# Performance work log

Measured on AMD Instinct MI355X. Metric: run time of the kernel, lower is better.

## Reference

```python
import jax, jax.numpy as jnp
import numpy as np

D_MODEL = 1024
N_HEADS = 16
D_HEAD = 64
D_FF = 4096
WINDOW = 256
B, T = 2, 2048


def setup_inputs() -> dict:
    key = jax.random.key(0)
    ks = jax.random.split(key, 10)
    tot = N_HEADS * D_HEAD
    def w(k, shape):
        # approximate kaiming_normal_ fan_out init: std = sqrt(2/fan_out)
        fan_out = shape[0]
        return jax.random.normal(k, shape, jnp.float32) * np.sqrt(2.0 / fan_out)
    return {
        "x": jax.random.normal(ks[0], (B, T, D_MODEL), jnp.float32),
        "ln1_w": jnp.ones((D_MODEL,), jnp.float32),
        "qkv_w": w(ks[1], (3 * tot, D_MODEL)),
        "gate_w": w(ks[2], (tot, D_MODEL)),
        "out_w": w(ks[3], (D_MODEL, tot)),
        "ln2_w": jnp.ones((D_MODEL,), jnp.float32),
        "wg": w(ks[4], (D_FF, D_MODEL)),
        "wu": w(ks[5], (D_FF, D_MODEL)),
        "wo": w(ks[6], (D_MODEL, D_FF)),
    }


def _rmsnorm(x, w):
    return x * jax.lax.rsqrt(jnp.mean(x * x, axis=-1, keepdims=True) + 1e-6) * w


def _attention(x, qkv_w, gate_w, out_w):
    Bq, Tq, _ = x.shape
    tot = N_HEADS * D_HEAD
    qkv = x @ qkv_w.T  # [B,T,3*tot]
    q, k, v = jnp.split(qkv, 3, axis=-1)
    q = q.reshape(Bq, Tq, N_HEADS, D_HEAD).transpose(0, 2, 1, 3)
    k = k.reshape(Bq, Tq, N_HEADS, D_HEAD).transpose(0, 2, 1, 3)
    v = v.reshape(Bq, Tq, N_HEADS, D_HEAD).transpose(0, 2, 1, 3)
    scale = D_HEAD ** -0.5
    scores = jnp.einsum("bhqd,bhkd->bhqk", q, k) * scale
    pos = jnp.arange(Tq)
    dist = pos[:, None] - pos[None, :]
    allowed = (dist >= 0) & (dist < WINDOW)  # causal sliding window
    mask = jnp.where(allowed, 0.0, -jnp.inf).astype(scores.dtype)
    attn = jax.nn.softmax(scores + mask[None, None], axis=-1)
    out = jnp.einsum("bhqk,bhkd->bhqd", attn, v)
    out = out.transpose(0, 2, 1, 3).reshape(Bq, Tq, tot)
    gate = jax.nn.sigmoid(x @ gate_w.T)
    return (out * gate) @ out_w.T


def reference(x, ln1_w, qkv_w, gate_w, out_w, ln2_w, wg, wu, wo):
    x = x + _attention(_rmsnorm(x, ln1_w), qkv_w, gate_w, out_w)
    h = _rmsnorm(x, ln2_w)
    ffn = (jax.nn.silu(h @ wg.T) * (h @ wu.T)) @ wo.T
    return x + ffn
```

## Files before the change

kernel.cpp:

```cpp
#include <hip/hip_runtime.h>


#define DEV __device__ __forceinline__

using u16 = unsigned short;
typedef __attribute__((ext_vector_type(8))) short  short8;
typedef __attribute__((ext_vector_type(4))) float  floatx4;

DEV u16 f2bf(float f) {
  unsigned u = __builtin_bit_cast(unsigned, f);
  u += 0x7FFFu + ((u >> 16) & 1u);
  return (u16)(u >> 16);
}
DEV float bf2f(u16 h) {
  unsigned u = ((unsigned)h) << 16;
  return __builtin_bit_cast(float, u);
}
DEV floatx4 mfma16(short8 a, short8 b, floatx4 c) {
  return __builtin_amdgcn_mfma_f32_16x16x32_bf16(a, b, c, 0, 0, 0);
}
DEV void gload16(const u16* g, const char* lds_base_wave_uniform) {
  __builtin_amdgcn_global_load_lds(
      (const __attribute__((address_space(1))) void*)g,
      (__attribute__((address_space(3))) void*)lds_base_wave_uniform,
      16, 0, 0);
}
#define WAITVM(n) asm volatile("s_waitcnt vmcnt(" #n ")" ::: "memory")
DEV void blockbar() {
  asm volatile("" ::: "memory");
  __builtin_amdgcn_s_barrier();
  asm volatile("" ::: "memory");
}

__global__ __launch_bounds__(256) void cvt_all_k(
    const float* __restrict__ s0, const float* __restrict__ s1,
    const float* __restrict__ s2, const float* __restrict__ s3,
    const float* __restrict__ s4, const float* __restrict__ s5,
    u16* __restrict__ d0, u16* __restrict__ d1, u16* __restrict__ d2,
    u16* __restrict__ d3, u16* __restrict__ d4, u16* __restrict__ d5) {
  const int b = blockIdx.x;
  const float* in; u16* out; int base;
  if (b < 3072)       { in = s0; out = d0; base = 0; }
  else if (b < 4096)  { in = s1; out = d1; base = 3072; }
  else if (b < 5120)  { in = s2; out = d2; base = 4096; }
  else if (b < 9216)  { in = s3; out = d3; base = 5120; }
  else if (b < 13312) { in = s4; out = d4; base = 9216; }
  else                { in = s5; out = d5; base = 13312; }
  const size_t i = (size_t)(b - base) * 256 + threadIdx.x;
  const float4 v = ((const float4*)in)[i];
  ushort4 r;
  r.x = f2bf(v.x); r.y = f2bf(v.y); r.z = f2bf(v.z); r.w = f2bf(v.w);
  ((ushort4*)out)[i] = r;
}

__global__ __launch_bounds__(256) void rmsnorm_k(const float* __restrict__ x,
                                                 const float* __restrict__ wt,
                                                 u16* __restrict__ o) {
  __shared__ float red[4];
  const int row = blockIdx.x;
  const int tid = threadIdx.x;
  const float4 v = ((const float4*)(x + (size_t)row * 1024))[tid];
  float ss = v.x * v.x + v.y * v.y + v.z * v.z + v.w * v.w;
  ss += __shfl_xor(ss, 1, 64);
  ss += __shfl_xor(ss, 2, 64);
  ss += __shfl_xor(ss, 4, 64);
  ss += __shfl_xor(ss, 8, 64);
  ss += __shfl_xor(ss, 16, 64);
  ss += __shfl_xor(ss, 32, 64);
  if ((tid & 63) == 0) red[tid >> 6] = ss;
  __syncthreads();
  const float tot = red[0] + red[1] + red[2] + red[3];
  const float sc = rsqrtf(tot * (1.0f / 1024.0f) + 1e-6f);
  const float4 wv = ((const float4*)wt)[tid];
  ushort4 r;
  r.x = f2bf(v.x * sc * wv.x);
  r.y = f2bf(v.y * sc * wv.y);
  r.z = f2bf(v.z * sc * wv.z);
  r.w = f2bf(v.w * sc * wv.w);
  ((ushort4*)(o + (size_t)row * 1024))[tid] = r;
}

template <int CFG, int EPI>
__global__ __launch_bounds__((CFG == 0) ? 512 : 256, 2) void gemm8p(
    const u16* __restrict__ Ag, const u16* __restrict__ Bg, int N, int K,
    u16* __restrict__ cb, float* __restrict__ cf,
    const u16* __restrict__ aux, const float* __restrict__ resid,
    u16* __restrict__ cb2) {
  constexpr int BM = (CFG == 0) ? 256 : 128;
  constexpr int NWAVES = (CFG == 0) ? 8 : 4;
  constexpr int WAVES_N = (CFG == 0) ? 4 : 2;
  constexpr int WM = (CFG == 0) ? 128 : 64;
  constexpr int NI = WM / 16;
  constexpr int NJ = 4;
  constexpr int IH = (CFG == 0) ? NI / 2 : NI;
  constexpr int GB = BM * 64;
  constexpr int BUFB = 4 * GB;
  __shared__ __align__(16) char lds[2 * BUFB];

  const int tid = threadIdx.x;
  const int w = tid >> 6, lane = tid & 63;
  const int wm = w / WAVES_N, wn = w % WAVES_N;
  const int g = lane >> 4, r16 = lane & 15;

  int bid = blockIdx.y * gridDim.x + blockIdx.x;
  const int cpx = (gridDim.x * gridDim.y) >> 3;
  bid = (bid & 7) * cpx + (bid >> 3);
  const int m0 = (bid / gridDim.x) * BM;
  const int n0 = (bid % gridDim.x) * BM;

  floatx4 acc[NI][NJ];
#pragma unroll
  for (int i = 0; i < NI; i++)
#pragma unroll
    for (int j = 0; j < NJ; j++) acc[i][j] = (floatx4){0.f, 0.f, 0.f, 0.f};

  const int nt = K >> 6;

  const int srow = w * 32 + (lane >> 2);
  const int scol8 = (lane & 3) * 8;
  auto stageG = [&](int G, int t) {
    if (t >= nt) return;
    const u16* Mat = (G < 2) ? Ag : Bg;
    const int base0 = (G < 2) ? m0 : n0;
    const int kc = t * 64 + (G & 1) * 32 + scol8;
    const char* dst = lds + (t & 1) * BUFB + G * GB + w * 2048;
#pragma unroll
    for (int q = 0; q < 2; q++)
      gload16(Mat + (size_t)(base0 + srow + q * 16) * K + kc, dst + q * 1024);
  };

  auto rdA = [&](short8* af, int ks, int ihalf, const char* buf) {
#pragma unroll
    for (int i = 0; i < IH; i++) {
      const int arow = wm * WM + (ihalf * IH + i) * 16 + r16;
      af[i] = *(const short8*)(buf + ks * GB + arow * 64 + g * 16);
    }
  };
  auto rdB = [&](short8* bf_, int ks, const char* buf) {
#pragma unroll
    for (int j = 0; j < NJ; j++) {
      const int brow = wn * 64 + j * 16 + r16;
      bf_[j] = *(const short8*)(buf + 2 * GB + ks * GB + brow * 64 + g * 16);
    }
  };
  auto mm = [&](short8* af, short8* bf_, int ihalf) {
    __builtin_amdgcn_s_setprio(1);
#pragma unroll
    for (int i = 0; i < IH; i++)
#pragma unroll
      for (int j = 0; j < NJ; j++)
        acc[ihalf * IH + i][j] = mfma16(af[i], bf_[j], acc[ihalf * IH + i][j]);
    __builtin_amdgcn_s_setprio(0);
  };

  if constexpr (CFG == 0) { stageG(1, 0); stageG(2, 0); stageG(0, 0); stageG(3, 0); }
  else                    { stageG(0, 0); stageG(2, 0); stageG(1, 0); stageG(3, 0); }

  for (int t = 0; t < nt; ++t) {
    const char* buf = lds + (t & 1) * BUFB;
    short8 af[IH], bfv[NJ];
    if constexpr (CFG == 0) {
      WAITVM(2);
      blockbar();
      rdA(af, 0, 0, buf); rdB(bfv, 0, buf);
      stageG(1, t + 1);
      mm(af, bfv, 0);
      blockbar();
      rdA(af, 0, 1, buf);
      stageG(2, t + 1);
      mm(af, bfv, 1);
      if (t + 1 < nt) { WAITVM(4); } else { WAITVM(0); }
      blockbar();
      rdA(af, 1, 0, buf); rdB(bfv, 1, buf);
      stageG(0, t + 1);
      mm(af, bfv, 0);
      blockbar();
      rdA(af, 1, 1, buf);
      stageG(3, t + 1);
      mm(af, bfv, 1);
    } else {
      WAITVM(4);
      blockbar();
      rdA(af, 0, 0, buf); rdB(bfv, 0, buf);
      stageG(0, t + 1); stageG(2, t + 1);
      mm(af, bfv, 0);
      if (t + 1 < nt) { WAITVM(4); } else { WAITVM(0); }
      blockbar();
      rdA(af, 1, 0, buf); rdB(bfv, 1, buf);
      stageG(1, t + 1); stageG(3, t + 1);
      mm(af, bfv, 0);
    }
  }

#pragma unroll
  for (int i = 0; i < NI; i++) {
    const int row = m0 + wm * WM + i * 16 + g * 4;
#pragma unroll
    for (int j = 0; j < NJ; j++) {
      const int col = n0 + wn * 64 + j * 16 + r16;
#pragma unroll
      for (int rr = 0; rr < 4; rr++) {
        const float v = acc[i][j][rr];
        if constexpr (EPI == 2) {
          cb[(size_t)(row + rr) * N + col] = f2bf(v / (1.0f + __expf(-v)));
        } else if constexpr (EPI == 3) {
          const size_t idx = (size_t)(row + rr) * N + col;
          cb[idx] = f2bf(v * bf2f(aux[idx]));
        } else if constexpr (EPI == 4) {
          const size_t idx = (size_t)(row + rr) * N + col;
          cf[idx] = v + resid[idx];
        } else if constexpr (EPI == 6) {
          if (col < 3072)
            cb[(size_t)(row + rr) * 3072 + col] = f2bf(v);
          else
            cb2[(size_t)(row + rr) * 1024 + (col - 3072)] =
                f2bf(1.0f / (1.0f + __expf(-v)));
        }
      }
    }
  }
}

__global__ __launch_bounds__(256) void attn_win_kernel(
    const u16* __restrict__ qkv, const u16* __restrict__ gate,
    u16* __restrict__ out) {
  __shared__ __align__(16) u16 Kl[64][80];
  __shared__ __align__(16) u16 Vt[64][80];
  __shared__ __align__(16) u16 Pl[4][16][80];

  const int tid = threadIdx.x;
  const int w = tid >> 6, lane = tid & 63;
  const int g = lane >> 4, r16 = lane & 15;

  const int q0 = blockIdx.x * 64;
  const int h = blockIdx.y;
  const int b = blockIdx.z;
  const u16* qb_ = qkv + (size_t)b * 2048 * 3072;

  const int tq = q0 + w * 16 + r16;
  const u16* qptr = qb_ + (size_t)tq * 3072 + h * 64;
  const short8 aq0 = *(const short8*)(qptr + g * 8);
  const short8 aq1 = *(const short8*)(qptr + 32 + g * 8);

  floatx4 O[4] = {{0,0,0,0},{0,0,0,0},{0,0,0,0},{0,0,0,0}};
  float mrow[4] = {-1e30f, -1e30f, -1e30f, -1e30f};
  float lrow[4] = {0.f, 0.f, 0.f, 0.f};

  const int srow = tid >> 2;
  const int sq4 = tid & 3;
  const int qw = q0 + w * 16;

  for (int kt = q0 - 256; kt <= q0; kt += 64) {
    if (kt < 0) continue;
    {
      const u16* kb = qb_ + (size_t)(kt + srow) * 3072 + 1024 + h * 64 + sq4 * 16;
      const short8 kv0 = *(const short8*)kb;
      const short8 kv1 = *(const short8*)(kb + 8);
      *(short8*)&Kl[srow][sq4 * 16] = kv0;
      *(short8*)&Kl[srow][sq4 * 16 + 8] = kv1;
      const u16* vb = kb + 1024;
      const short8 vv0 = *(const short8*)vb;
      const short8 vv1 = *(const short8*)(vb + 8);
#pragma unroll
      for (int j = 0; j < 8; j++) Vt[sq4 * 16 + j][srow] = (u16)vv0[j];
#pragma unroll
      for (int j = 0; j < 8; j++) Vt[sq4 * 16 + 8 + j][srow] = (u16)vv1[j];
    }
    __syncthreads();

    const bool active = (qw + 15 >= kt) && (qw - kt < 319);
    if (active) {
      floatx4 S[4];
#pragma unroll
      for (int nf = 0; nf < 4; nf++) {
        const short8 bk0 = *(const short8*)&Kl[nf * 16 + r16][g * 8];
        const short8 bk1 = *(const short8*)&Kl[nf * 16 + r16][32 + g * 8];
        floatx4 a = {0.f, 0.f, 0.f, 0.f};
        a = mfma16(aq0, bk0, a);
        a = mfma16(aq1, bk1, a);
        S[nf] = a;
      }
      float pm[4][4];
      float nmax[4] = {-1e30f, -1e30f, -1e30f, -1e30f};
#pragma unroll
      for (int nf = 0; nf < 4; nf++) {
        const int key = kt + nf * 16 + r16;
#pragma unroll
        for (int rr = 0; rr < 4; rr++) {
          const int q = qw + g * 4 + rr;
          const int dist = q - key;
          const float s = (dist >= 0 && dist < 256) ? S[nf][rr] : -1e30f;
          pm[nf][rr] = s;
          nmax[rr] = fmaxf(nmax[rr], s);
        }
      }
#pragma unroll
      for (int rr = 0; rr < 4; rr++) {
        float v = nmax[rr];
        v = fmaxf(v, __shfl_xor(v, 1, 64));
        v = fmaxf(v, __shfl_xor(v, 2, 64));
        v = fmaxf(v, __shfl_xor(v, 4, 64));
        v = fmaxf(v, __shfl_xor(v, 8, 64));
        const float mnew = fmaxf(mrow[rr], v);
        const float alpha = __expf(0.125f * (mrow[rr] - mnew));
        mrow[rr] = mnew;
        lrow[rr] *= alpha;
#pragma unroll
        for (int n = 0; n < 4; n++) O[n][rr] *= alpha;
        float ls = 0.f;
#pragma unroll
        for (int nf = 0; nf < 4; nf++) {
          const float s = pm[nf][rr];
          const float pv = (s < -1e29f) ? 0.f : __expf(0.125f * (s - mnew));
          pm[nf][rr] = pv;
          ls += pv;
        }
        ls += __shfl_xor(ls, 1, 64);
        ls += __shfl_xor(ls, 2, 64);
        ls += __shfl_xor(ls, 4, 64);
        ls += __shfl_xor(ls, 8, 64);
        lrow[rr] += ls;
      }
#pragma unroll
      for (int nf = 0; nf < 4; nf++)
#pragma unroll
        for (int rr = 0; rr < 4; rr++)
          Pl[w][g * 4 + rr][nf * 16 + r16] = f2bf(pm[nf][rr]);
#pragma unroll
      for (int kf = 0; kf < 2; kf++) {
        const short8 pa = *(const short8*)&Pl[w][r16][kf * 32 + g * 8];
#pragma unroll
        for (int n = 0; n < 4; n++) {
          const short8 vb8 = *(const short8*)&Vt[n * 16 + r16][kf * 32 + g * 8];
          O[n] = mfma16(pa, vb8, O[n]);
        }
      }
    }
    __syncthreads();
  }

#pragma unroll
  for (int n = 0; n < 4; n++) {
#pragma unroll
    for (int rr = 0; rr < 4; rr++) {
      const int t = qw + g * 4 + rr;
      const size_t idx = ((size_t)(b * 2048 + t)) * 1024 + h * 64 + n * 16 + r16;
      const float gv = bf2f(gate[idx]);
      const float ov = (O[n][rr] / lrow[rr]) * gv;
      out[idx] = f2bf(ov);
    }
  }
}

extern "C" void kernel_launch(void* const* d_in, const int* in_sizes, int n_in,
                              void* d_out, int out_size, void* d_ws,
                              size_t ws_size, hipStream_t stream) {
  (void)in_sizes; (void)n_in; (void)out_size; (void)ws_size;
  const float* x     = (const float*)d_in[0];
  const float* ln1   = (const float*)d_in[1];
  const float* qkvw  = (const float*)d_in[2];
  const float* gatew = (const float*)d_in[3];
  const float* outw  = (const float*)d_in[4];
  const float* ln2   = (const float*)d_in[5];
  const float* wg    = (const float*)d_in[6];
  const float* wu    = (const float*)d_in[7];
  const float* wo    = (const float*)d_in[8];
  float* outp = (float*)d_out;

  u16* p = (u16*)d_ws;
  u16* qkvw_b  = p; p += 3 * 1024 * 1024;
  u16* gatew_b = p; p += 1024 * 1024;
  u16* outw_b  = p; p += 1024 * 1024;
  u16* wg_b    = p; p += 4 * 1024 * 1024;
  u16* wu_b    = p; p += 4 * 1024 * 1024;
  u16* wo_b    = p; p += 4 * 1024 * 1024;
  u16* xn      = p; p += 4096 * 1024;
  u16* qkvb    = p; p += (size_t)4096 * 3072;
  u16* gates   = p; p += 4096 * 1024;
  u16* a3      = p; p += 4096 * 1024;
  u16* hb      = p; p += 4096 * 1024;
  u16* gs      = p; p += (size_t)4096 * 4096;
  float* x2    = (float*)p;

  cvt_all_k<<<17408, 256, 0, stream>>>(qkvw, gatew, outw, wg, wu, wo,
                                       qkvw_b, gatew_b, outw_b, wg_b, wu_b, wo_b);

  rmsnorm_k<<<4096, 256, 0, stream>>>(x, ln1, xn);

  gemm8p<0, 6><<<dim3(16, 16), 512, 0, stream>>>(
      xn, qkvw_b, 4096, 1024, qkvb, nullptr, nullptr, nullptr, gates);

  attn_win_kernel<<<dim3(32, 16, 2), 256, 0, stream>>>(qkvb, gates, a3);

  gemm8p<1, 4><<<dim3(8, 32), 256, 0, stream>>>(
      a3, outw_b, 1024, 1024, nullptr, x2, nullptr, x, nullptr);

  rmsnorm_k<<<4096, 256, 0, stream>>>(x2, ln2, hb);

  gemm8p<0, 2><<<dim3(16, 16), 512, 0, stream>>>(
      hb, wg_b, 4096, 1024, gs, nullptr, nullptr, nullptr, nullptr);
  gemm8p<0, 3><<<dim3(16, 16), 512, 0, stream>>>(
      hb, wu_b, 4096, 1024, gs, nullptr, gs, nullptr, nullptr);

  gemm8p<1, 4><<<dim3(8, 32), 256, 0, stream>>>(
      gs, wo_b, 1024, 4096, nullptr, outp, nullptr, x2, nullptr);
}
```

Before: 364.7 us.

## Swizzle GEMM LDS layout and use 8 waves for 128-tile config

Applies an XOR swizzle to the k-group column of LDS tiles for both staging writes and fragment reads, to cut LDS bank conflicts in the MFMA operand loads. The 128x128 GEMM config now runs 8 waves (512 threads), each owning a 64x32 sub-tile. Staging is reorganised so each wave loads 16 rows per pass, and the vmcnt waits and stage order are adjusted to match. More waves per tile aim to hide latency better, at the cost of fewer accumulators per wave and more staging instructions per byte.

```diff
diff --git a/kernel.cpp b/kernel.cpp
--- a/kernel.cpp
+++ b/kernel.cpp
@@ -81,26 +81,27 @@
 }
 
 template <int CFG, int EPI>
-__global__ __launch_bounds__((CFG == 0) ? 512 : 256, 2) void gemm8p(
+__global__ __launch_bounds__(512, 2) void gemm8p(
     const u16* __restrict__ Ag, const u16* __restrict__ Bg, int N, int K,
     u16* __restrict__ cb, float* __restrict__ cf,
     const u16* __restrict__ aux, const float* __restrict__ resid,
     u16* __restrict__ cb2) {
   constexpr int BM = (CFG == 0) ? 256 : 128;
-  constexpr int NWAVES = (CFG == 0) ? 8 : 4;
-  constexpr int WAVES_N = (CFG == 0) ? 4 : 2;
   constexpr int WM = (CFG == 0) ? 128 : 64;
+  constexpr int WN = (CFG == 0) ? 64 : 32;
   constexpr int NI = WM / 16;
-  constexpr int NJ = 4;
+  constexpr int NJ = WN / 16;
   constexpr int IH = (CFG == 0) ? NI / 2 : NI;
   constexpr int GB = BM * 64;
+  constexpr int QI = (CFG == 0) ? 2 : 1;
   constexpr int BUFB = 4 * GB;
   __shared__ __align__(16) char lds[2 * BUFB];
 
   const int tid = threadIdx.x;
   const int w = tid >> 6, lane = tid & 63;
-  const int wm = w / WAVES_N, wn = w % WAVES_N;
+  const int wm = w >> 2, wn = w & 3;
   const int g = lane >> 4, r16 = lane & 15;
+  const int gx = (g ^ ((r16 >> 1) & 3)) << 4;
 
   int bid = blockIdx.y * gridDim.x + blockIdx.x;
   const int cpx = (gridDim.x * gridDim.y) >> 3;
@@ -116,31 +117,32 @@
 
   const int nt = K >> 6;
 
-  const int srow = w * 32 + (lane >> 2);
-  const int scol8 = (lane & 3) * 8;
+  const int kg_src = (lane & 3) ^ ((lane >> 3) & 3);
   auto stageG = [&](int G, int t) {
     if (t >= nt) return;
     const u16* Mat = (G < 2) ? Ag : Bg;
-    const int base0 = (G < 2) ? m0 : n0;
-    const int kc = t * 64 + (G & 1) * 32 + scol8;
-    const char* dst = lds + (t & 1) * BUFB + G * GB + w * 2048;
-#pragma unroll
-    for (int q = 0; q < 2; q++)
-      gload16(Mat + (size_t)(base0 + srow + q * 16) * K + kc, dst + q * 1024);
+    const int b0 = (G < 2) ? m0 : n0;
+    const int kc = t * 64 + (G & 1) * 32 + kg_src * 8;
+    const char* dst = lds + (t & 1) * BUFB + G * GB + w * 1024;
+#pragma unroll
+    for (int q = 0; q < QI; q++) {
+      const int row = q * 128 + w * 16 + (lane >> 2);
+      gload16(Mat + (size_t)(b0 + row) * K + kc, dst + q * 8192);
+    }
   };
 
   auto rdA = [&](short8* af, int ks, int ihalf, const char* buf) {
 #pragma unroll
     for (int i = 0; i < IH; i++) {
       const int arow = wm * WM + (ihalf * IH + i) * 16 + r16;
-      af[i] = *(const short8*)(buf + ks * GB + arow * 64 + g * 16);
+      af[i] = *(const short8*)(buf + ks * GB + arow * 64 + gx);
     }
   };
   auto rdB = [&](short8* bf_, int ks, const char* buf) {
 #pragma unroll
     for (int j = 0; j < NJ; j++) {
-      const int brow = wn * 64 + j * 16 + r16;
-      bf_[j] = *(const short8*)(buf + 2 * GB + ks * GB + brow * 64 + g * 16);
+      const int brow = wn * WN + j * 16 + r16;
+      bf_[j] = *(const short8*)(buf + 2 * GB + ks * GB + brow * 64 + gx);
     }
   };
   auto mm = [&](short8* af, short8* bf_, int ihalf) {
@@ -153,17 +155,16 @@
     __builtin_amdgcn_s_setprio(0);
   };
 
-  if constexpr (CFG == 0) { stageG(1, 0); stageG(2, 0); stageG(0, 0); stageG(3, 0); }
-  else                    { stageG(0, 0); stageG(2, 0); stageG(1, 0); stageG(3, 0); }
+  stageG(0, 0); stageG(2, 0); stageG(1, 0); stageG(3, 0);
 
   for (int t = 0; t < nt; ++t) {
     const char* buf = lds + (t & 1) * BUFB;
     short8 af[IH], bfv[NJ];
     if constexpr (CFG == 0) {
-      WAITVM(2);
+      WAITVM(4);
       blockbar();
       rdA(af, 0, 0, buf); rdB(bfv, 0, buf);
-      stageG(1, t + 1);
+      stageG(0, t + 1);
       mm(af, bfv, 0);
       blockbar();
       rdA(af, 0, 1, buf);
@@ -172,19 +173,19 @@
       if (t + 1 < nt) { WAITVM(4); } else { WAITVM(0); }
       blockbar();
       rdA(af, 1, 0, buf); rdB(bfv, 1, buf);
-      stageG(0, t + 1);
+      stageG(1, t + 1);
       mm(af, bfv, 0);
       blockbar();
       rdA(af, 1, 1, buf);
       stageG(3, t + 1);
       mm(af, bfv, 1);
     } else {
-      WAITVM(4);
+      WAITVM(2);
       blockbar();
       rdA(af, 0, 0, buf); rdB(bfv, 0, buf);
       stageG(0, t + 1); stageG(2, t + 1);
       mm(af, bfv, 0);
-      if (t + 1 < nt) { WAITVM(4); } else { WAITVM(0); }
+      if (t + 1 < nt) { WAITVM(2); } else { WAITVM(0); }
       blockbar();
       rdA(af, 1, 0, buf); rdB(bfv, 1, buf);
       stageG(1, t + 1); stageG(3, t + 1);
@@ -197,7 +198,7 @@
     const int row = m0 + wm * WM + i * 16 + g * 4;
 #pragma unroll
     for (int j = 0; j < NJ; j++) {
-      const int col = n0 + wn * 64 + j * 16 + r16;
+      const int col = n0 + wn * WN + j * 16 + r16;
 #pragma unroll
       for (int rr = 0; rr < 4; rr++) {
         const float v = acc[i][j][rr];
@@ -392,7 +393,7 @@
 
   attn_win_kernel<<<dim3(32, 16, 2), 256, 0, stream>>>(qkvb, gates, a3);
 
-  gemm8p<1, 4><<<dim3(8, 32), 256, 0, stream>>>(
+  gemm8p<1, 4><<<dim3(8, 32), 512, 0, stream>>>(
       a3, outw_b, 1024, 1024, nullptr, x2, nullptr, x, nullptr);
 
   rmsnorm_k<<<4096, 256, 0, stream>>>(x2, ln2, hb);
@@ -402,6 +403,6 @@
   gemm8p<0, 3><<<dim3(16, 16), 512, 0, stream>>>(
       hb, wu_b, 4096, 1024, gs, nullptr, gs, nullptr, nullptr);
 
-  gemm8p<1, 4><<<dim3(8, 32), 256, 0, stream>>>(
+  gemm8p<1, 4><<<dim3(8, 32), 512, 0, stream>>>(
       gs, wo_b, 1024, 4096, nullptr, outp, nullptr, x2, nullptr);
 }
```

New measurement: 360.0 us. No clear change (-1.3%).
